# Optimization experiments

Measured on AMD Instinct MI355X. Metric: run time of the kernel, lower is better.

Reference implementation:

```python
import jax, jax.numpy as jnp
import numpy as np

B, L, D, K = 8, 4096, 1024, 2048  # batch, seq_len, hidden, max selected tokens


def setup_inputs() -> dict:
    key = jax.random.key(0)
    k1, k2 = jax.random.split(key)
    hidden_states = jax.random.normal(k1, (B, L, D), dtype=jnp.float32)
    # boundary_mask with exactly K True per row so next_max_seqlen == K is static
    scores = jax.random.uniform(k2, (B, L))
    order = jnp.argsort(scores, axis=1)  # random permutation per row
    boundary_mask = jnp.zeros((B, L), dtype=bool)
    rows = jnp.arange(B)[:, None]
    boundary_mask = boundary_mask.at[rows, order[:, :K]].set(True)
    mask = jnp.ones((B, L), dtype=bool)
    return {
        "hidden_states": hidden_states,
        "boundary_mask": boundary_mask,
        "mask": mask,
        "next_max_seqlen": K,
    }


def reference(hidden_states, boundary_mask, mask, next_max_seqlen):
    # Padded path of ChunkLayer.forward (mask is provided, cu_seqlens=None).
    Bn, Ln, Dn = hidden_states.shape
    num_tokens = boundary_mask.sum(axis=-1)  # [B]
    # boundary tokens keep their position; non-boundary tokens pushed past L
    token_idx = jnp.arange(Ln)[None, :] + (~boundary_mask).astype(jnp.int32) * Ln
    seq_sorted_indices = jnp.argsort(token_idx, axis=1)  # stable sort, [B, L]
    idx = seq_sorted_indices[:, :next_max_seqlen, None]  # [B, K, 1]
    next_hidden_states = jnp.take_along_axis(hidden_states, idx, axis=1)  # [B, K, D]
    next_mask = jnp.arange(next_max_seqlen)[None, :] < num_tokens[:, None]  # [B, K]
    return next_hidden_states, next_mask
```

## Files before the change

kernel.cpp:

```cpp
#include <hip/hip_runtime.h>

#define BB 8
#define LL 4096
#define DD 1024
#define KK 2048

#define RPB 8
#define NWORDS (LL / 64)

typedef float f32x4 __attribute__((ext_vector_type(4)));

__global__ void __launch_bounds__(256)
fused_gather_kernel(const f32x4* __restrict__ src,
                    const int* __restrict__ bm,
                    f32x4* __restrict__ dst,
                    float* __restrict__ om) {
    __shared__ unsigned long long words[NWORDS];
    __shared__ int pre[NWORDS];
    __shared__ int srows[RPB];

    const int blk   = blockIdx.x;
    const int tid   = threadIdx.x;
    const int lane  = tid & 63;
    const int wave  = tid >> 6;
    const int b     = blk >> 8;
    const int kbase = (blk & 255) * RPB;

    const int* m = bm + (size_t)b * LL;

#pragma unroll
    for (int j = 0; j < 16; ++j) {
        const unsigned long long w = __ballot(m[j * 256 + tid] != 0);
        if (lane == 0) {
            const int wi = j * 4 + wave;
            words[wi] = w;
            pre[wi]   = __popcll(w);
        }
    }
    __syncthreads();

    if (wave == 0) {
        int v = pre[lane];
#pragma unroll
        for (int off = 1; off < 64; off <<= 1) {
            const int t = __shfl_up(v, off, 64);
            if (lane >= off) v += t;
        }
        pre[lane] = v;
    }
    __syncthreads();

    const int total = pre[NWORDS - 1];

    if (tid < RPB) {
        const int kb = kbase + tid;
        int lo = 0, hi = NWORDS - 1, r;
        unsigned long long x;
        if (kb < total) {
            while (lo < hi) { const int mid = (lo + hi) >> 1; if (pre[mid] > kb) hi = mid; else lo = mid + 1; }
            r = kb - ((lo == 0) ? 0 : pre[lo - 1]);
            x = words[lo];
        } else {
            const int rz = kb - total;
            while (lo < hi) { const int mid = (lo + hi) >> 1; if ((mid + 1) * 64 - pre[mid] > rz) hi = mid; else lo = mid + 1; }
            r = rz - (lo * 64 - ((lo == 0) ? 0 : pre[lo - 1]));
            x = ~words[lo];
        }
        int pos = 0;
#pragma unroll
        for (int sh = 32; sh >= 1; sh >>= 1) {
            const int c = __popcll(x & ((1ull << sh) - 1ull));
            if (r >= c) { r -= c; x >>= sh; pos += sh; }
        }
        srows[tid] = lo * 64 + pos;
        om[(size_t)b * KK + kb] = (kb < total) ? 1.0f : 0.0f;
    }
    __syncthreads();

    const size_t srcbase = (size_t)b * LL * (DD / 4);
    const size_t dstbase = ((size_t)b * KK + kbase) * (DD / 4);
#pragma unroll
    for (int j = 0; j < RPB; ++j) {
        const f32x4 v = __builtin_nontemporal_load(&src[srcbase + (size_t)srows[j] * (DD / 4) + tid]);
        __builtin_nontemporal_store(v, &dst[dstbase + (size_t)j * (DD / 4) + tid]);
    }
}

extern "C" void kernel_launch(void* const* d_in, const int* in_sizes, int n_in,
                              void* d_out, int out_size, void* d_ws, size_t ws_size,
                              hipStream_t stream) {
    const float* hs = (const float*)d_in[0];
    const int*   bm = (const int*)d_in[1];

    float* out_hs   = (float*)d_out;
    float* out_mask = (float*)d_out + (size_t)BB * KK * DD;

    fused_gather_kernel<<<(BB * KK) / RPB, 256, 0, stream>>>(
        (const f32x4*)hs, bm, (f32x4*)out_hs, out_mask);
}
```

Before: 29.20 us.

## Assign rows per wave, drop shared-row sync, batch loads before stores

Each block now handles 16 output rows instead of 8, so the blocks that recompute the mask ballot and prefix scan are halved. Each wave resolves its own 4 source rows in lanes 0-3 and broadcasts them with shuffles, which removes the shared srows array and the final __syncthreads. All 16 float4 loads are issued before any stores to raise memory-level parallelism. The cost is more registers per thread and fewer blocks in flight.

```diff
diff --git a/kernel.cpp b/kernel.cpp
--- a/kernel.cpp
+++ b/kernel.cpp
@@ -5,7 +5,7 @@
 #define DD 1024
 #define KK 2048
 
-#define RPB 8
+#define RPB 16
 #define NWORDS (LL / 64)
 
 typedef float f32x4 __attribute__((ext_vector_type(4)));
@@ -17,14 +17,13 @@
                     float* __restrict__ om) {
     __shared__ unsigned long long words[NWORDS];
     __shared__ int pre[NWORDS];
-    __shared__ int srows[RPB];
 
     const int blk   = blockIdx.x;
     const int tid   = threadIdx.x;
     const int lane  = tid & 63;
     const int wave  = tid >> 6;
-    const int b     = blk >> 8;
-    const int kbase = (blk & 255) * RPB;
+    const int b     = blk >> 7;
+    const int kbase = (blk & 127) * RPB;
 
     const int* m = bm + (size_t)b * LL;
 
@@ -52,8 +51,12 @@
 
     const int total = pre[NWORDS - 1];
 
-    if (tid < RPB) {
-        const int kb = kbase + tid;
+    if (tid < RPB)
+        om[(size_t)b * KK + kbase + tid] = (kbase + tid < total) ? 1.0f : 0.0f;
+
+    int srow = 0;
+    if (lane < 4) {
+        const int kb = kbase + wave * 4 + lane;
         int lo = 0, hi = NWORDS - 1, r;
         unsigned long long x;
         if (kb < total) {
@@ -72,17 +75,26 @@
             const int c = __popcll(x & ((1ull << sh) - 1ull));
             if (r >= c) { r -= c; x >>= sh; pos += sh; }
         }
-        srows[tid] = lo * 64 + pos;
-        om[(size_t)b * KK + kb] = (kb < total) ? 1.0f : 0.0f;
+        srow = lo * 64 + pos;
     }
-    __syncthreads();
+    int rows[4];
+#pragma unroll
+    for (int q = 0; q < 4; ++q) rows[q] = __shfl(srow, q, 64);
 
-    const size_t srcbase = (size_t)b * LL * (DD / 4);
-    const size_t dstbase = ((size_t)b * KK + kbase) * (DD / 4);
+    f32x4 v[16];
 #pragma unroll
-    for (int j = 0; j < RPB; ++j) {
-        const f32x4 v = __builtin_nontemporal_load(&src[srcbase + (size_t)srows[j] * (DD / 4) + tid]);
-        __builtin_nontemporal_store(v, &dst[dstbase + (size_t)j * (DD / 4) + tid]);
+    for (int q = 0; q < 4; ++q) {
+        const f32x4* s = src + ((size_t)b * LL + rows[q]) * (DD / 4) + lane;
+#pragma unroll
+        for (int it = 0; it < 4; ++it)
+            v[q * 4 + it] = __builtin_nontemporal_load(&s[it * 64]);
+    }
+    f32x4* d = dst + ((size_t)b * KK + kbase + wave * 4) * (DD / 4) + lane;
+#pragma unroll
+    for (int q = 0; q < 4; ++q) {
+#pragma unroll
+        for (int it = 0; it < 4; ++it)
+            __builtin_nontemporal_store(v[q * 4 + it], &d[q * (DD / 4) + it * 64]);
     }
 }
 
```

Result: slower. 30.50 us (+4.5%).
